# Performance work log

Hardware: AMD Instinct MI355X
Metric: run time of the kernel (lower is better)

The kernel has to match this reference:

```python
import jax, jax.numpy as jnp
import numpy as np

K = 3  # filter_size
PAD = (K - 1) // 2


def setup_inputs() -> dict:
    key = jax.random.key(0)
    k1, k2, k3 = jax.random.split(key, 3)
    B, C, H, Wd = 4, 256, 128, 128
    x = jax.random.normal(k1, (B, C, H, Wd), dtype=jnp.float32)
    # 1x1 conv params: out_channels = C * K^2
    W = jax.random.normal(k2, (C * K * K, C), dtype=jnp.float32) * (1.0 / np.sqrt(C))
    b = jax.random.normal(k3, (C * K * K,), dtype=jnp.float32) * 0.01
    return {"x": x, "W": W, "b": b}


def _extract_patches(x):
    # x: (B,C,H,W) -> (B,C,H,W,K*K), kernel positions row-major (matches F.unfold)
    B, C, H, Wd = x.shape
    xp = jnp.pad(x, ((0, 0), (0, 0), (PAD, PAD), (PAD, PAD)))
    patches = jnp.stack(
        [xp[:, :, i:i + H, j:j + Wd] for i in range(K) for j in range(K)],
        axis=-1,
    )
    return patches


def reference(x, W, b):
    B, C, H, Wd = x.shape
    # 1x1 conv: (B,C,H,W) x (C*K^2, C) -> (B, C*K^2, H, W)
    filters = jnp.einsum('bchw,oc->bohw', x, W) + b[None, :, None, None]
    # view(B, C, K^2, H, W) then permute to (B,C,H,W,K^2)
    filters = filters.reshape(B, C, K * K, H, Wd).transpose(0, 1, 3, 4, 2)
    patches = _extract_patches(x)  # (B,C,H,W,K^2), unfold ordering c-major then pos
    return jnp.sum(patches * filters, axis=-1)  # (B,C,H,W)
```

## Files before the change

### kernel.cpp

```cpp
#include <hip/hip_runtime.h>


typedef __attribute__((ext_vector_type(8))) short bf16x8;
typedef __attribute__((ext_vector_type(4))) float f32x4;

__device__ __forceinline__ unsigned int f2bf(float f) {
    unsigned int u = __float_as_uint(f);
    return (u + 0x7fffu + ((u >> 16) & 1u)) >> 16;
}
__device__ __forceinline__ unsigned int pack2(float a, float b) {
    return f2bf(a) | (f2bf(b) << 16);
}

__global__ __launch_bounds__(256) void wconv_kernel(const float* __restrict__ W,
                                                    unsigned char* __restrict__ Wb) {
    int idx = blockIdx.x * 256 + threadIdx.x;
    int o = idx >> 5, g = idx & 31;
    const float4* src = (const float4*)(W + ((size_t)o << 8) + ((size_t)g << 3));
    float4 v0 = src[0], v1 = src[1];
    uint4 pk;
    pk.x = pack2(v0.x, v0.y); pk.y = pack2(v0.z, v0.w);
    pk.z = pack2(v1.x, v1.y); pk.w = pack2(v1.z, v1.w);
    int kh = g >> 4, g2 = g & 15, s = g2 >> 2, q = g2 & 3;
    int chunk = o / 144, oo = o - chunk * 144;
    int ni = oo >> 4, lrow = oo & 15;
    int j = kh * 3 + ni / 3, ni_ = ni % 3;
    size_t dst = (size_t)chunk * 73728 + (size_t)j * 12288
               + (size_t)(s * 3 + ni_) * 1024 + (size_t)((q << 4) + lrow) * 16;
    *(uint4*)(Wb + dst) = pk;
}


#define SYNC_VM(N) asm volatile("s_waitcnt vmcnt(" #N ") lgkmcnt(0)\n\ts_barrier" ::: "memory")
#define SYNC_LG    asm volatile("s_waitcnt lgkmcnt(0)\n\ts_barrier" ::: "memory")
#define WAIT_LGKM0 asm volatile("s_waitcnt lgkmcnt(0)" ::: "memory")
#define FENCE      asm volatile("" ::: "memory")

#define STAGE(CH, J)                                                            \
    do {                                                                        \
        const int sl_ = (wv < 6) ? wv : (wv - 6);                               \
        const unsigned char* bs_ = Wb + (size_t)(CH) * 73728                    \
            + (size_t)(J) * 12288 + sl_ * 2048 + (lane << 4);                   \
        unsigned char* bd_ = smem + ((J) % 4) * 12288 + sl_ * 2048;             \
        __builtin_amdgcn_global_load_lds(                                       \
            (const __attribute__((address_space(1))) void*)(bs_),               \
            (__attribute__((address_space(3))) void*)(bd_), 16, 0, 0);          \
        __builtin_amdgcn_global_load_lds(                                       \
            (const __attribute__((address_space(1))) void*)(bs_ + 1024),        \
            (__attribute__((address_space(3))) void*)(bd_ + 1024), 16, 0, 0);   \
    } while (0)

#define MFMA_SUB(J)                                                             \
    do {                                                                        \
        const int kh_ = (J) / 3, snib_ = ((J) % 3) * 3;                         \
        const unsigned char* bb_ = smem + ((J) % 4) * 12288 + (lane << 4);      \
        _Pragma("unroll")                                                       \
        for (int s_ = 0; s_ < 4; ++s_) {                                        \
            const bf16x8 a0_ = afr[(kh_ << 2) + s_];                            \
            const bf16x8 a1_ = afr[8 + (kh_ << 2) + s_];                        \
            _Pragma("unroll")                                                   \
            for (int ni_ = 0; ni_ < 3; ++ni_) {                                 \
                const bf16x8 bq_ = *(const bf16x8*)(bb_ + ((s_ * 3 + ni_) << 10)); \
                acc[0][snib_ + ni_] = __builtin_amdgcn_mfma_f32_16x16x32_bf16(  \
                    a0_, bq_, acc[0][snib_ + ni_], 0, 0, 0);                    \
                acc[1][snib_ + ni_] = __builtin_amdgcn_mfma_f32_16x16x32_bf16(  \
                    a1_, bq_, acc[1][snib_ + ni_], 0, 0, 0);                    \
            }                                                                   \
        }                                                                       \
    } while (0)

__global__ __launch_bounds__(512, 2) void dfgemm_kernel(
        const unsigned char* __restrict__ Wb, const float* __restrict__ x,
        const float* __restrict__ bias, float* __restrict__ out) {
    __shared__ __align__(16) unsigned char smem[122880];

    const int t = threadIdx.x;
    const int lane = t & 63, wv = t >> 6;
    const int quad = lane >> 4, lrow = lane & 15;

    const int b = blockIdx.x >> 6;
    const int hp = blockIdx.x & 63;
    const int h = (hp << 1) + (wv >> 2);
    const int wq = wv & 3;

    STAGE(0, 0); STAGE(0, 1); STAGE(0, 2); STAGE(0, 3);

    bf16x8 afr[16];
    {
        const float* xrow = x + ((size_t)b << 22) + (h << 7);
        #pragma unroll
        for (int mi = 0; mi < 2; ++mi) {
            const int w = (wq << 5) + (mi << 4) + lrow;
            #pragma unroll
            for (int gg = 0; gg < 8; ++gg) {
                const float* p = xrow + ((size_t)((gg << 5) + (quad << 3)) << 14) + w;
                float v[8];
                #pragma unroll
                for (int e = 0; e < 8; ++e) v[e] = p[(size_t)e << 14];
                uint4 pk;
                pk.x = pack2(v[0], v[1]); pk.y = pack2(v[2], v[3]);
                pk.z = pack2(v[4], v[5]); pk.w = pack2(v[6], v[7]);
                afr[(mi << 3) + gg] = *(const bf16x8*)&pk;
            }
        }
    }
    SYNC_VM(0);

    #pragma unroll 1
    for (int chunk = 0; chunk < 16; ++chunk) {
        const int c1 = (chunk + 1) & 15;
        f32x4 acc[2][9];
        const f32x4 zero = {0.f, 0.f, 0.f, 0.f};
        #pragma unroll
        for (int mi = 0; mi < 2; ++mi)
            #pragma unroll
            for (int ni = 0; ni < 9; ++ni) acc[mi][ni] = zero;

        SYNC_VM(8);
        MFMA_SUB(0);

        SYNC_VM(8);
        STAGE(chunk, 4);
        MFMA_SUB(1);

        SYNC_VM(8);
        STAGE(chunk, 5);
        MFMA_SUB(2);

        SYNC_VM(8);
        STAGE(c1, 2);
        MFMA_SUB(3);

        SYNC_VM(4);
        STAGE(c1, 3);
        MFMA_SUB(4);

        SYNC_VM(4);
        STAGE(c1, 0);
        MFMA_SUB(5);

        SYNC_LG;
        STAGE(c1, 1);
        FENCE;

        float* Y = (float*)(smem + 49152 + wv * 9216);
        #pragma unroll
        for (int half = 0; half < 2; ++half) {
            #pragma unroll
            for (int ni = 0; ni < 9; ++ni) {
                const int o = (ni << 4) + lrow;
                *(f32x4*)(Y + (o << 4) + ((quad ^ (lrow & 3)) << 2)) = acc[half][ni];
            }
            WAIT_LGKM0;

            const int w = (wq << 5) + (half << 4) + lrow;
            #pragma unroll
            for (int it = 0; it < 4; ++it) {
                const int cgl = (it << 2) + quad;
                const int cg = (chunk << 4) + cgl;
                const int ob = cgl * 9;
                const float* bp = bias + cg * 9;
                const float* xc = x + ((size_t)((b << 8) + cg) << 14);
                float sum = 0.f;
                #pragma unroll
                for (int p = 0; p < 9; ++p) {
                    const int o = ob + p;
                    const float yv = Y[(o << 4) + (lrow ^ ((o & 3) << 2))];
                    const int hh = h + p / 3 - 1, ww = w + p % 3 - 1;
                    float xv = 0.f;
                    if ((unsigned)hh < 128u && (unsigned)ww < 128u)
                        xv = xc[(hh << 7) + ww];
                    sum += (yv + bp[p]) * xv;
                }
                out[((size_t)((b << 8) + cg) << 14) + (h << 7) + w] = sum;
            }
        }
    }
}

extern "C" void kernel_launch(void* const* d_in, const int* in_sizes, int n_in,
                              void* d_out, int out_size, void* d_ws, size_t ws_size,
                              hipStream_t stream) {
    const float* x    = (const float*)d_in[0];
    const float* W    = (const float*)d_in[1];
    const float* bias = (const float*)d_in[2];
    float* out = (float*)d_out;

    unsigned char* Wb = (unsigned char*)d_ws;

    wconv_kernel<<<288, 256, 0, stream>>>(W, Wb);
    dfgemm_kernel<<<256, 512, 0, stream>>>(Wb, x, bias, out);
}
```

Baseline: 225.3 us.

## Permute weight rows and swap MFMA operands to skip LDS transpose of accumulators

The weight preprocessing now permutes output rows so that, after swapping the A/B operands of the MFMA, each lane's accumulator registers already hold the nine filter taps for its own channels and pixel. The epilogue reads filter values straight from registers instead of writing accumulators to shared memory and reading them back transposed. This removes the LDS store/load round trip and its wait, and shrinks shared memory from about 120KB to 48KB, which could allow more resident blocks. The register indexing into acc must resolve at compile time through full unrolling, or the accumulators may spill.

```diff
diff --git a/kernel.cpp b/kernel.cpp
--- a/kernel.cpp
+++ b/kernel.cpp
@@ -14,26 +14,28 @@
 
 __global__ __launch_bounds__(256) void wconv_kernel(const float* __restrict__ W,
                                                     unsigned char* __restrict__ Wb) {
-    int idx = blockIdx.x * 256 + threadIdx.x;
-    int o = idx >> 5, g = idx & 31;
+    int idx0 = blockIdx.x * 256 + threadIdx.x;
+    int o = idx0 >> 5, g = idx0 & 31;
     const float4* src = (const float4*)(W + ((size_t)o << 8) + ((size_t)g << 3));
     float4 v0 = src[0], v1 = src[1];
     uint4 pk;
     pk.x = pack2(v0.x, v0.y); pk.y = pack2(v0.z, v0.w);
     pk.z = pack2(v1.x, v1.y); pk.w = pack2(v1.z, v1.w);
-    int kh = g >> 4, g2 = g & 15, s = g2 >> 2, q = g2 & 3;
-    int chunk = o / 144, oo = o - chunk * 144;
-    int ni = oo >> 4, lrow = oo & 15;
-    int j = kh * 3 + ni / 3, ni_ = ni % 3;
-    size_t dst = (size_t)chunk * 73728 + (size_t)j * 12288
-               + (size_t)(s * 3 + ni_) * 1024 + (size_t)((q << 4) + lrow) * 16;
+    int kh = g >> 4, g2 = g & 15, s = g2 >> 2, kq = g2 & 3;
+    int chunk = o / 144, oc = o - chunk * 144;
+    int c_local = oc / 9, p = oc - c_local * 9;
+    int q = c_local >> 2, c4 = c_local & 3;
+    int idx = c4 * 9 + p;
+    int ni = idx >> 2, j = idx & 3, r = (q << 2) + j;
+    int jsub = kh * 3 + ni / 3, ni_ = ni % 3;
+    size_t dst = (size_t)chunk * 73728 + (size_t)jsub * 12288
+               + (size_t)(s * 3 + ni_) * 1024 + (size_t)((kq << 4) + r) * 16;
     *(uint4*)(Wb + dst) = pk;
 }
 
 
 #define SYNC_VM(N) asm volatile("s_waitcnt vmcnt(" #N ") lgkmcnt(0)\n\ts_barrier" ::: "memory")
 #define SYNC_LG    asm volatile("s_waitcnt lgkmcnt(0)\n\ts_barrier" ::: "memory")
-#define WAIT_LGKM0 asm volatile("s_waitcnt lgkmcnt(0)" ::: "memory")
 #define FENCE      asm volatile("" ::: "memory")
 
 #define STAGE(CH, J)                                                            \
@@ -62,9 +64,9 @@
             for (int ni_ = 0; ni_ < 3; ++ni_) {                                 \
                 const bf16x8 bq_ = *(const bf16x8*)(bb_ + ((s_ * 3 + ni_) << 10)); \
                 acc[0][snib_ + ni_] = __builtin_amdgcn_mfma_f32_16x16x32_bf16(  \
-                    a0_, bq_, acc[0][snib_ + ni_], 0, 0, 0);                    \
+                    bq_, a0_, acc[0][snib_ + ni_], 0, 0, 0);                    \
                 acc[1][snib_ + ni_] = __builtin_amdgcn_mfma_f32_16x16x32_bf16(  \
-                    a1_, bq_, acc[1][snib_ + ni_], 0, 0, 0);                    \
+                    bq_, a1_, acc[1][snib_ + ni_], 0, 0, 0);                    \
             }                                                                   \
         }                                                                       \
     } while (0)
@@ -72,7 +74,7 @@
 __global__ __launch_bounds__(512, 2) void dfgemm_kernel(
         const unsigned char* __restrict__ Wb, const float* __restrict__ x,
         const float* __restrict__ bias, float* __restrict__ out) {
-    __shared__ __align__(16) unsigned char smem[122880];
+    __shared__ __align__(16) unsigned char smem[49152];
 
     const int t = threadIdx.x;
     const int lane = t & 63, wv = t >> 6;
@@ -143,29 +145,20 @@
         STAGE(c1, 1);
         FENCE;
 
-        float* Y = (float*)(smem + 49152 + wv * 9216);
         #pragma unroll
-        for (int half = 0; half < 2; ++half) {
+        for (int mi = 0; mi < 2; ++mi) {
+            const int w = (wq << 5) + (mi << 4) + lrow;
             #pragma unroll
-            for (int ni = 0; ni < 9; ++ni) {
-                const int o = (ni << 4) + lrow;
-                *(f32x4*)(Y + (o << 4) + ((quad ^ (lrow & 3)) << 2)) = acc[half][ni];
-            }
-            WAIT_LGKM0;
-
-            const int w = (wq << 5) + (half << 4) + lrow;
-            #pragma unroll
-            for (int it = 0; it < 4; ++it) {
-                const int cgl = (it << 2) + quad;
-                const int cg = (chunk << 4) + cgl;
-                const int ob = cgl * 9;
+            for (int c4 = 0; c4 < 4; ++c4) {
+                const int cg = (chunk << 4) + (quad << 2) + c4;
                 const float* bp = bias + cg * 9;
                 const float* xc = x + ((size_t)((b << 8) + cg) << 14);
                 float sum = 0.f;
                 #pragma unroll
                 for (int p = 0; p < 9; ++p) {
-                    const int o = ob + p;
-                    const float yv = Y[(o << 4) + (lrow ^ ((o & 3) << 2))];
+                    const int idx = c4 * 9 + p;
+                    const int ni = idx >> 2, j = idx & 3;
+                    const float yv = acc[mi][ni][j];
                     const int hh = h + p / 3 - 1, ww = w + p % 3 - 1;
                     float xv = 0.f;
                     if ((unsigned)hh < 128u && (unsigned)ww < 128u)
```

Result: faster. 213.8 us (-5.1%).
